# Kernel tuning notes

Measured on AMD Instinct MI355X. Metric: run time of the kernel, lower is better.

Reference implementation:

```python
import jax, jax.numpy as jnp
import numpy as np

NQ = 10      # num_qubits
NL = 3       # num_layers
EPS = 1e-5   # BatchNorm1d eps

# PennyLane gate conventions (wire 0 = most significant bit of the state index)

def _mat_ry(t):
    c, s = jnp.cos(t / 2), jnp.sin(t / 2)
    r0 = jnp.stack([c, -s], -1)
    r1 = jnp.stack([s, c], -1)
    return jnp.stack([r0, r1], -2).astype(jnp.complex64)

def _mat_rx(t):
    c, s = jnp.cos(t / 2), jnp.sin(t / 2)
    c = c.astype(jnp.complex64)
    js = (-1j) * s.astype(jnp.complex64)
    r0 = jnp.stack([c, js], -1)
    r1 = jnp.stack([js, c], -1)
    return jnp.stack([r0, r1], -2)

def _mat_rz(t):
    em = jnp.exp(-0.5j * t.astype(jnp.complex64))
    ep = jnp.exp(0.5j * t.astype(jnp.complex64))
    z = jnp.zeros_like(em)
    r0 = jnp.stack([em, z], -1)
    r1 = jnp.stack([z, ep], -1)
    return jnp.stack([r0, r1], -2)

def _apply_1q(state, U, q):
    # state: (B, 2**NQ); U: (2,2) shared or (B,2,2) per-sample
    B = state.shape[0]
    s = state.reshape(B, 2 ** q, 2, -1)
    if U.ndim == 3:
        s = jnp.einsum('bij,bajc->baic', U, s)
    else:
        s = jnp.einsum('ij,bajc->baic', U, s)
    return s.reshape(B, -1)

def _cnot(state, c, t):
    # control c < target t: flip target bit where control bit == 1
    B = state.shape[0]
    s = state.reshape(B, 2 ** c, 2, 2 ** (t - c - 1), 2, -1)
    s = jnp.stack([s[:, :, 0], s[:, :, 1, :, ::-1, :]], axis=2)
    return s.reshape(B, -1)

def _circuit(x, params):
    # batched statevector simulation of the full circuit
    B = x.shape[0]
    state = jnp.zeros((B, 2 ** NQ), jnp.complex64).at[:, 0].set(1.0)
    for q in range(NQ):                       # RY encoding (per-sample angles)
        state = _apply_1q(state, _mat_ry(x[:, q]), q)
    for l in range(NL):
        for q in range(NQ):                   # RZ, RX, RY trainable rotations
            state = _apply_1q(state, _mat_rz(params[l, q, 0]), q)
            state = _apply_1q(state, _mat_rx(params[l, q, 1]), q)
            state = _apply_1q(state, _mat_ry(params[l, q, 2]), q)
        for i in range(NQ - 1):               # 'full' entanglement: CNOT chain
            state = _cnot(state, i, i + 1)
    probs = state.real ** 2 + state.imag ** 2
    exps = []
    for q in range(NQ):                       # <Z_q> = P(bit_q=0) - P(bit_q=1)
        p = probs.reshape(B, 2 ** q, 2, -1).sum(axis=(1, 3))
        exps.append(p[:, 0] - p[:, 1])
    return jnp.stack(exps, axis=1)            # (B, NQ)

def setup_inputs() -> dict:
    key = jax.random.key(0)
    k1, k2 = jax.random.split(key)
    x = jax.random.normal(k1, (16384, NQ), jnp.float32)
    params = jax.random.normal(k2, (NL, NQ, 3), jnp.float32)
    gamma = jnp.ones((NQ,), jnp.float32)
    beta = jnp.zeros((NQ,), jnp.float32)
    return {"x": x, "params": params, "gamma": gamma, "beta": beta}

def reference(x, params, gamma, beta):
    out = _circuit(x, params)
    # BatchNorm1d in training mode (biased batch variance)
    mean = out.mean(axis=0)
    var = ((out - mean) ** 2).mean(axis=0)
    return gamma * (out - mean) * jax.lax.rsqrt(var + EPS) + beta
```

## Files before the change

kernel.cpp:

```cpp
#include <hip/hip_runtime.h>
#include <hip/hip_fp16.h>

#define NQ 10
#define NSAMP 16384
#define BN_EPS 1e-5f

union H2U { __half2 h; unsigned u; };
__device__ __forceinline__ __half2 u2h(unsigned u) { H2U t; t.u = u; return t.h; }
__device__ __forceinline__ unsigned h2u(__half2 h) { H2U t; t.h = h; return t.u; }
__device__ __forceinline__ __half2 hswap(__half2 x) { return __lowhigh2highlow(x); }
__device__ __forceinline__ __half2 hpack(float lo, float hi) {
  return __floats2half2_rn(lo, hi);
}

template<int M>
__device__ __forceinline__ unsigned shufu(unsigned v, int a30, int a28, int a20) {
  if constexpr (M < 32) {
    return (unsigned)__builtin_amdgcn_ds_swizzle((int)v, (M << 10) | 0x1F);
  } else {
    const int addr = (M == 0x30) ? a30 : (M == 0x28) ? a28 : a20;
    return (unsigned)__builtin_amdgcn_ds_bpermute(addr, (int)v);
  }
}
template<int M>
__device__ __forceinline__ __half2 shufh(__half2 v, int a30, int a28, int a20) {
  return u2h(shufu<M>(h2u(v), a30, a28, a20));
}

constexpr int ML_[3][10] = {
  {0x20,0x10,0x08,0x04,0x02,0x01, 0,   0,   0,   0},
  {0x30,0x18,0x0C,0x06,0x03,0x01, 0,   0,   0,   0},
  {0x28,0x14,0x0A,0x05,0x02,0x01, 0,   0,   0,   0}};
constexpr int MR_[3][10] = {
  {0,0,0,0,0,0,   0x8,0x4,0x2,0x1},
  {0,0,0,0,0,0x8, 0xC,0x6,0x3,0x1},
  {0,0,0,0,0x8,0x4,0xA,0x5,0x2,0x1}};
constexpr int HR_[3][10] = {
  {0,0,0,0,0,0, 0x8,0x4,0x2,0x1},
  {0,0,0,0,0,0, 0x8,0xC,0xE,0xF},
  {0,0,0,0,0,0, 0x8,0x4,0xA,0x5}};
constexpr int EHL[10] = {0x20,0x30,0x18,0x0C,0x26,0x33,0x19,0x0C,0x26,0x33};

constexpr int SMASK[12] = {0x20,0x30,0x38,0x3C,0x3E,0x3F, 0x20,0x10,0x28,0x14,0x2A,0x15};
constexpr int SIX[2][10] = {{0,1,2,3,4,5,5,5,5,5}, {6,7,8,9,10,11,10,11,10,11}};

constexpr bool par4(int v) { return ((v >> 3 & 1) ^ (v >> 2 & 1) ^ (v >> 1 & 1) ^ (v & 1)) != 0; }

__device__ __forceinline__ void updh(__half2& ar, __half2& ai, __half2 br, __half2 bi,
                                     __half2 WR, __half2 AWI, __half2 NAWI,
                                     __half2 AVR, __half2 VI, __half2 NVI) {
  const __half2 a0r = ar, a0i = ai;
  ar = __hfma2(WR, a0r, __hfma2(AWI, a0i, __hfma2(AVR, br, __hmul2(NVI, bi))));
  ai = __hfma2(WR, a0i, __hfma2(NAWI, a0r, __hfma2(AVR, bi, __hmul2(VI, br))));
}

template<int ML, int MR, int HR>
__device__ __forceinline__ void gateh(__half2* __restrict__ Hr, __half2* __restrict__ Hi,
                                      unsigned sgnw, int a30, int a28, int a20, uint4 cp) {
  const unsigned swi = cp.y ^ sgnw;
  const unsigned svr = cp.z ^ sgnw;
  constexpr unsigned hif = (HR & 8) ? 0x80000000u : 0u;
  const __half2 WR  = u2h(cp.x);
  const __half2 VI  = u2h(cp.w);
  const __half2 NVI = u2h(cp.w ^ 0x80008000u);
  const __half2 WI0 = u2h(swi ^ hif);
  const __half2 WI1 = u2h(swi ^ hif ^ 0x80008000u);
  const __half2 NWI0 = WI1, NWI1 = WI0;
  const __half2 VR0 = u2h(svr ^ hif);
  const __half2 VR1 = u2h(svr ^ hif ^ 0x80008000u);

  if constexpr (MR == 0) {
    #pragma unroll
    for (int j = 0; j < 8; ++j) {
      const __half2 br = shufh<ML>(Hr[j], a30, a28, a20);
      const __half2 bi = shufh<ML>(Hi[j], a30, a28, a20);
      const bool cp_ = par4(j & (HR & 7));
      updh(Hr[j], Hi[j], br, bi, WR, cp_ ? WI1 : WI0, cp_ ? NWI1 : NWI0,
           cp_ ? VR1 : VR0, VI, NVI);
    }
  } else if constexpr ((MR & 7) == 0) {
    #pragma unroll
    for (int j = 0; j < 8; ++j) {
      __half2 br = Hr[j], bi = Hi[j];
      if constexpr (ML != 0) { br = shufh<ML>(br, a30, a28, a20); bi = shufh<ML>(bi, a30, a28, a20); }
      br = hswap(br); bi = hswap(bi);
      const bool cp_ = par4(j & (HR & 7));
      updh(Hr[j], Hi[j], br, bi, WR, cp_ ? WI1 : WI0, cp_ ? NWI1 : NWI0,
           cp_ ? VR1 : VR0, VI, NVI);
    }
  } else {
    constexpr int JX = MR & 7;
    constexpr int HB = (JX >= 4) ? 4 : (JX >= 2) ? 2 : 1;
    #pragma unroll
    for (int j = 0; j < 8; ++j) {
      if (!(j & HB)) {
        const int j2 = j ^ JX;
        __half2 bra = Hr[j2], bia = Hi[j2], brb = Hr[j], bib = Hi[j];
        if constexpr (ML != 0) {
          bra = shufh<ML>(bra, a30, a28, a20); bia = shufh<ML>(bia, a30, a28, a20);
          brb = shufh<ML>(brb, a30, a28, a20); bib = shufh<ML>(bib, a30, a28, a20);
        }
        if constexpr ((MR & 8) != 0) {
          bra = hswap(bra); bia = hswap(bia); brb = hswap(brb); bib = hswap(bib);
        }
        const bool cpa = par4(j & (HR & 7));
        updh(Hr[j], Hi[j], bra, bia, WR, cpa ? WI1 : WI0, cpa ? NWI1 : NWI0,
             cpa ? VR1 : VR0, VI, NVI);
        const bool cpb = par4(j2 & (HR & 7));
        updh(Hr[j2], Hi[j2], brb, bib, WR, cpb ? WI1 : WI0, cpb ? NWI1 : NWI0,
             cpb ? VR1 : VR0, VI, NVI);
      }
    }
  }
}

template<int L, int Q>
__device__ __forceinline__ void rotgh(const uint4* __restrict__ cph, __half2* Hr, __half2* Hi,
                                      const unsigned* __restrict__ sgnv,
                                      int a30, int a28, int a20) {
  const uint4 cp = cph[(L - 1) * 10 + Q];
  gateh<ML_[L][Q], MR_[L][Q], HR_[L][Q]>(Hr, Hi, sgnv[SIX[L - 1][Q]], a30, a28, a20, cp);
}

__device__ __forceinline__ void enc2(const float4 g, float xq,
                                     float& ar, float& ai, float& br, float& bi) {
  const float t = xq * 0.5f;
  const float sq = __sinf(t), cq = __cosf(t);
  ar = g.x * cq - g.z * sq;
  ai = g.y * cq + g.w * sq;
  br = g.z * cq + g.x * sq;
  bi = g.w * cq - g.y * sq;
}
__device__ __forceinline__ void cmul(float& zr, float& zi,
                                     float xr, float xi, float yr, float yi) {
  zr = xr * yr - xi * yi;
  zi = xr * yi + xi * yr;
}

__global__ void coef_kernel(const float* __restrict__ params, float* __restrict__ coef,
                            unsigned* __restrict__ cph, float* __restrict__ stats) {
  int g = threadIdx.x;
  if (g < 20) stats[g] = 0.f;
  if (g < 30) {
    float t0 = params[g * 3 + 0] * 0.5f;
    float t1 = params[g * 3 + 1] * 0.5f;
    float t2 = params[g * 3 + 2] * 0.5f;
    float sa, ca, s2, c2, s3, c3;
    __sincosf(t0, &sa, &ca);
    __sincosf(t1, &s2, &c2);
    __sincosf(t2, &s3, &c3);
    float A = c3 * c2, Bv = s3 * s2, C = s3 * c2, D = c3 * s2;
    float wr = A * ca + Bv * sa;
    float wi = Bv * ca - A * sa;
    float vr = C * ca - D * sa;
    float vi = -(C * sa + D * ca);
    coef[g * 4 + 0] = wr;
    coef[g * 4 + 1] = wi;
    coef[g * 4 + 2] = vr;
    coef[g * 4 + 3] = vi;
    if (g >= 10) {
      int gi = g - 10;
      cph[gi * 4 + 0] = h2u(hpack(wr, wr));
      cph[gi * 4 + 1] = h2u(hpack(wi, wi));
      cph[gi * 4 + 2] = h2u(hpack(vr, vr));
      cph[gi * 4 + 3] = h2u(hpack(vi, vi));
    }
  }
}

__global__ __launch_bounds__(256) void circuit_kernel(const float* __restrict__ x,
                                                      const float* __restrict__ coef,
                                                      const uint4* __restrict__ cph,
                                                      float* __restrict__ out,
                                                      float* __restrict__ stats) {
  const int lane = threadIdx.x & 63;
  const int wv = threadIdx.x >> 6;
  const int wid = __builtin_amdgcn_readfirstlane(
      (int)((blockIdx.x * blockDim.x + threadIdx.x) >> 6));
  const float4* cg = (const float4*)coef;

  const int a30 = (lane ^ 0x30) << 2;
  const int a28 = (lane ^ 0x28) << 2;
  const int a20 = (lane ^ 0x20) << 2;

  unsigned sgnv[12];
  #pragma unroll
  for (int k = 0; k < 12; ++k)
    sgnv[k] = (__builtin_popcount(lane & SMASK[k]) & 1) ? 0u : 0x80008000u;

  const float* xrow = x + wid * NQ;
  float lr, li;
  {
    float ar, ai, br, bi;
    enc2(cg[0], xrow[0], ar, ai, br, bi);
    lr = (lane & 32) ? br : ar;
    li = (lane & 32) ? bi : ai;
  }
  #pragma unroll
  for (int q = 1; q < 6; ++q) {
    float ar, ai, br, bi;
    enc2(cg[q], xrow[q], ar, ai, br, bi);
    const int bit = 1 << (5 - q);
    const float tr = (lane & bit) ? br : ar;
    const float ti = (lane & bit) ? bi : ai;
    const float nr = lr * tr - li * ti;
    const float ni = lr * ti + li * tr;
    lr = nr; li = ni;
  }
  float sr[16], si[16];
  {
    float ar, ai, br, bi;
    float t2r[2], t2i[2], t4r[4], t4i[4], t8r[8], t8i[8];
    enc2(cg[6], xrow[6], ar, ai, br, bi);
    cmul(t2r[0], t2i[0], lr, li, ar, ai);
    cmul(t2r[1], t2i[1], lr, li, br, bi);
    enc2(cg[7], xrow[7], ar, ai, br, bi);
    #pragma unroll
    for (int j = 0; j < 2; ++j) {
      cmul(t4r[2*j+0], t4i[2*j+0], t2r[j], t2i[j], ar, ai);
      cmul(t4r[2*j+1], t4i[2*j+1], t2r[j], t2i[j], br, bi);
    }
    enc2(cg[8], xrow[8], ar, ai, br, bi);
    #pragma unroll
    for (int j = 0; j < 4; ++j) {
      cmul(t8r[2*j+0], t8i[2*j+0], t4r[j], t4i[j], ar, ai);
      cmul(t8r[2*j+1], t8i[2*j+1], t4r[j], t4i[j], br, bi);
    }
    enc2(cg[9], xrow[9], ar, ai, br, bi);
    #pragma unroll
    for (int j = 0; j < 8; ++j) {
      cmul(sr[2*j+0], si[2*j+0], t8r[j], t8i[j], ar, ai);
      cmul(sr[2*j+1], si[2*j+1], t8r[j], t8i[j], br, bi);
    }
  }
  __half2 Hr[8], Hi[8];
  #pragma unroll
  for (int j = 0; j < 8; ++j) {
    Hr[j] = hpack(sr[j], sr[j | 8]);
    Hi[j] = hpack(si[j], si[j | 8]);
  }

  rotgh<1,0>(cph,Hr,Hi,sgnv,a30,a28,a20); rotgh<1,1>(cph,Hr,Hi,sgnv,a30,a28,a20);
  rotgh<1,2>(cph,Hr,Hi,sgnv,a30,a28,a20); rotgh<1,3>(cph,Hr,Hi,sgnv,a30,a28,a20);
  rotgh<1,4>(cph,Hr,Hi,sgnv,a30,a28,a20); rotgh<1,5>(cph,Hr,Hi,sgnv,a30,a28,a20);
  rotgh<1,6>(cph,Hr,Hi,sgnv,a30,a28,a20); rotgh<1,7>(cph,Hr,Hi,sgnv,a30,a28,a20);
  rotgh<1,8>(cph,Hr,Hi,sgnv,a30,a28,a20); rotgh<1,9>(cph,Hr,Hi,sgnv,a30,a28,a20);

  rotgh<2,0>(cph,Hr,Hi,sgnv,a30,a28,a20); rotgh<2,1>(cph,Hr,Hi,sgnv,a30,a28,a20);
  rotgh<2,2>(cph,Hr,Hi,sgnv,a30,a28,a20); rotgh<2,3>(cph,Hr,Hi,sgnv,a30,a28,a20);
  rotgh<2,4>(cph,Hr,Hi,sgnv,a30,a28,a20); rotgh<2,5>(cph,Hr,Hi,sgnv,a30,a28,a20);
  rotgh<2,6>(cph,Hr,Hi,sgnv,a30,a28,a20); rotgh<2,7>(cph,Hr,Hi,sgnv,a30,a28,a20);
  rotgh<2,8>(cph,Hr,Hi,sgnv,a30,a28,a20); rotgh<2,9>(cph,Hr,Hi,sgnv,a30,a28,a20);

  __half2 A0 = u2h(0u), A1 = A0, A2 = A0, A3 = A0;
  #pragma unroll
  for (int j = 0; j < 8; ++j) {
    const __half2 P = __hfma2(Hr[j], Hr[j], __hmul2(Hi[j], Hi[j]));
    A0 = __hadd2(A0, P);
    A1 = par4(j & 4) ? __hsub2(A1, P) : __hadd2(A1, P);
    A2 = par4(j & 6) ? __hsub2(A2, P) : __hadd2(A2, P);
    A3 = par4(j & 3) ? __hsub2(A3, P) : __hadd2(A3, P);
  }
  const float a0lo = __half2float(__low2half(A0)), a0hi = __half2float(__high2half(A0));
  const float a1lo = __half2float(__low2half(A1)), a1hi = __half2float(__high2half(A1));
  const float a2lo = __half2float(__low2half(A2)), a2hi = __half2float(__high2half(A2));
  const float a3lo = __half2float(__low2half(A3)), a3hi = __half2float(__high2half(A3));
  const float tot = a0lo + a0hi;
  const float s8  = a0lo - a0hi;
  const float sc  = a1lo - a1hi;
  const float s6  = a2lo + a2hi;
  const float s3  = a3lo + a3hi;

  const float S[10] = {tot, tot, tot, tot, tot, tot, s8, sc, s6, s3};
  __half2 E[5];
  #pragma unroll
  for (int k = 0; k < 5; ++k) {
    float ea = S[2 * k], eb = S[2 * k + 1];
    ea = (__builtin_popcount(lane & EHL[2 * k]) & 1) ? -ea : ea;
    eb = (__builtin_popcount(lane & EHL[2 * k + 1]) & 1) ? -eb : eb;
    E[k] = hpack(ea, eb);
  }
  #pragma unroll
  for (int k = 0; k < 5; ++k) {
    E[k] = __hadd2(E[k], shufh<0x20>(E[k], a30, a28, a20));
    E[k] = __hadd2(E[k], shufh<0x10>(E[k], a30, a28, a20));
    E[k] = __hadd2(E[k], shufh<0x08>(E[k], a30, a28, a20));
    E[k] = __hadd2(E[k], shufh<0x04>(E[k], a30, a28, a20));
    E[k] = __hadd2(E[k], shufh<0x02>(E[k], a30, a28, a20));
    E[k] = __hadd2(E[k], shufh<0x01>(E[k], a30, a28, a20));
  }

  __shared__ float red[4][20];
  if (lane == 0) {
    #pragma unroll
    for (int k = 0; k < 5; ++k) {
      const float ea = __half2float(__low2half(E[k]));
      const float eb = __half2float(__high2half(E[k]));
      out[wid * NQ + 2 * k]     = ea;
      out[wid * NQ + 2 * k + 1] = eb;
      red[wv][2 * k]          = ea;
      red[wv][2 * k + 1]      = eb;
      red[wv][10 + 2 * k]     = ea * ea;
      red[wv][10 + 2 * k + 1] = eb * eb;
    }
  }
  __syncthreads();
  const int tid = threadIdx.x;
  if (tid < 20) {
    float ssum = red[0][tid] + red[1][tid] + red[2][tid] + red[3][tid];
    atomicAdd(&stats[tid], ssum);
  }
}

__global__ __launch_bounds__(256) void bn_kernel(float* __restrict__ out,
                                                 const float* __restrict__ stats,
                                                 const float* __restrict__ gamma,
                                                 const float* __restrict__ beta) {
  int i = blockIdx.x * 256 + threadIdx.x;
  if (i < NSAMP * NQ) {
    int q = i % NQ;
    float mean = stats[q] * (1.f / NSAMP);
    float var = stats[10 + q] * (1.f / NSAMP) - mean * mean;
    if (var < 0.f) var = 0.f;
    float rstd = rsqrtf(var + BN_EPS);
    float v = out[i];
    out[i] = gamma[q] * (v - mean) * rstd + beta[q];
  }
}

extern "C" void kernel_launch(void* const* d_in, const int* in_sizes, int n_in,
                              void* d_out, int out_size, void* d_ws, size_t ws_size,
                              hipStream_t stream) {
  const float* x      = (const float*)d_in[0];
  const float* params = (const float*)d_in[1];
  const float* gamma  = (const float*)d_in[2];
  const float* beta   = (const float*)d_in[3];
  float* out = (float*)d_out;
  float* stats = (float*)d_ws;
  float* coef = (float*)d_ws + 32;
  unsigned* cph = (unsigned*)((float*)d_ws + 160);

  coef_kernel<<<1, 32, 0, stream>>>(params, coef, cph, stats);
  circuit_kernel<<<NSAMP / 4, 256, 0, stream>>>(x, coef, (const uint4*)cph, out, stats);
  bn_kernel<<<(NSAMP * NQ + 255) / 256, 256, 0, stream>>>(out, stats, gamma, beta);
}
```

Baseline: 70.93 us.

## Pack two samples per wavefront in half2 lanes instead of splitting one state

Each wavefront now simulates two samples at once: the low and high halves of every half2 register hold the same amplitude index for sample A and sample B, and each lane keeps 16 registers instead of 8. This removes the in-register half swaps used when a gate paired the packed halves, and drops the special sign handling for the high half. The grid is halved. In exchange each lane holds twice as many state registers and builds two encoded states, and the final reduction shuffles ten packed values instead of five.

```diff
diff --git a/kernel.cpp b/kernel.cpp
--- a/kernel.cpp
+++ b/kernel.cpp
@@ -4,11 +4,11 @@
 #define NQ 10
 #define NSAMP 16384
 #define BN_EPS 1e-5f
+#define SGN 0x80008000u
 
 union H2U { __half2 h; unsigned u; };
 __device__ __forceinline__ __half2 u2h(unsigned u) { H2U t; t.u = u; return t.h; }
 __device__ __forceinline__ unsigned h2u(__half2 h) { H2U t; t.h = h; return t.u; }
-__device__ __forceinline__ __half2 hswap(__half2 x) { return __lowhigh2highlow(x); }
 __device__ __forceinline__ __half2 hpack(float lo, float hi) {
   return __floats2half2_rn(lo, hi);
 }
@@ -44,6 +44,9 @@
 constexpr int SMASK[12] = {0x20,0x30,0x38,0x3C,0x3E,0x3F, 0x20,0x10,0x28,0x14,0x2A,0x15};
 constexpr int SIX[2][10] = {{0,1,2,3,4,5,5,5,5,5}, {6,7,8,9,10,11,10,11,10,11}};
 
+constexpr int hibit4(int m) {
+  return m >= 8 ? 8 : (m >= 4 ? 4 : (m >= 2 ? 2 : (m ? 1 : 0)));
+}
 constexpr bool par4(int v) { return ((v >> 3 & 1) ^ (v >> 2 & 1) ^ (v >> 1 & 1) ^ (v & 1)) != 0; }
 
 __device__ __forceinline__ void updh(__half2& ar, __half2& ai, __half2 br, __half2 bi,
@@ -59,63 +62,50 @@
                                       unsigned sgnw, int a30, int a28, int a20, uint4 cp) {
   const unsigned swi = cp.y ^ sgnw;
   const unsigned svr = cp.z ^ sgnw;
-  constexpr unsigned hif = (HR & 8) ? 0x80000000u : 0u;
   const __half2 WR  = u2h(cp.x);
   const __half2 VI  = u2h(cp.w);
-  const __half2 NVI = u2h(cp.w ^ 0x80008000u);
-  const __half2 WI0 = u2h(swi ^ hif);
-  const __half2 WI1 = u2h(swi ^ hif ^ 0x80008000u);
-  const __half2 NWI0 = WI1, NWI1 = WI0;
-  const __half2 VR0 = u2h(svr ^ hif);
-  const __half2 VR1 = u2h(svr ^ hif ^ 0x80008000u);
+  const __half2 NVI = u2h(cp.w ^ SGN);
+  const __half2 WI0 = u2h(swi);
+  const __half2 WI1 = u2h(swi ^ SGN);
+  const __half2 VR0 = u2h(svr);
+  const __half2 VR1 = u2h(svr ^ SGN);
 
   if constexpr (MR == 0) {
     #pragma unroll
-    for (int j = 0; j < 8; ++j) {
-      const __half2 br = shufh<ML>(Hr[j], a30, a28, a20);
-      const __half2 bi = shufh<ML>(Hi[j], a30, a28, a20);
-      const bool cp_ = par4(j & (HR & 7));
-      updh(Hr[j], Hi[j], br, bi, WR, cp_ ? WI1 : WI0, cp_ ? NWI1 : NWI0,
-           cp_ ? VR1 : VR0, VI, NVI);
-    }
-  } else if constexpr ((MR & 7) == 0) {
-    #pragma unroll
-    for (int j = 0; j < 8; ++j) {
-      __half2 br = Hr[j], bi = Hi[j];
-      if constexpr (ML != 0) { br = shufh<ML>(br, a30, a28, a20); bi = shufh<ML>(bi, a30, a28, a20); }
-      br = hswap(br); bi = hswap(bi);
-      const bool cp_ = par4(j & (HR & 7));
-      updh(Hr[j], Hi[j], br, bi, WR, cp_ ? WI1 : WI0, cp_ ? NWI1 : NWI0,
-           cp_ ? VR1 : VR0, VI, NVI);
+    for (int r = 0; r < 16; ++r) {
+      const __half2 br = shufh<ML>(Hr[r], a30, a28, a20);
+      const __half2 bi = shufh<ML>(Hi[r], a30, a28, a20);
+      const bool p = par4(r & HR);
+      updh(Hr[r], Hi[r], br, bi, WR, p ? WI1 : WI0, p ? WI0 : WI1,
+           p ? VR1 : VR0, VI, NVI);
     }
   } else {
-    constexpr int JX = MR & 7;
-    constexpr int HB = (JX >= 4) ? 4 : (JX >= 2) ? 2 : 1;
+    constexpr int HB = hibit4(MR);
     #pragma unroll
-    for (int j = 0; j < 8; ++j) {
-      if (!(j & HB)) {
-        const int j2 = j ^ JX;
-        __half2 bra = Hr[j2], bia = Hi[j2], brb = Hr[j], bib = Hi[j];
+    for (int r = 0; r < 16; ++r) {
+      if (!(r & HB)) {
+        const int r2 = r ^ MR;
+        __half2 b0r, b0i, b1r, b1i;
         if constexpr (ML != 0) {
-          bra = shufh<ML>(bra, a30, a28, a20); bia = shufh<ML>(bia, a30, a28, a20);
-          brb = shufh<ML>(brb, a30, a28, a20); bib = shufh<ML>(bib, a30, a28, a20);
+          b0r = shufh<ML>(Hr[r2], a30, a28, a20); b0i = shufh<ML>(Hi[r2], a30, a28, a20);
+          b1r = shufh<ML>(Hr[r],  a30, a28, a20); b1i = shufh<ML>(Hi[r],  a30, a28, a20);
+        } else {
+          b0r = Hr[r2]; b0i = Hi[r2]; b1r = Hr[r]; b1i = Hi[r];
         }
-        if constexpr ((MR & 8) != 0) {
-          bra = hswap(bra); bia = hswap(bia); brb = hswap(brb); bib = hswap(bib);
-        }
-        const bool cpa = par4(j & (HR & 7));
-        updh(Hr[j], Hi[j], bra, bia, WR, cpa ? WI1 : WI0, cpa ? NWI1 : NWI0,
-             cpa ? VR1 : VR0, VI, NVI);
-        const bool cpb = par4(j2 & (HR & 7));
-        updh(Hr[j2], Hi[j2], brb, bib, WR, cpb ? WI1 : WI0, cpb ? NWI1 : NWI0,
-             cpb ? VR1 : VR0, VI, NVI);
+        const bool pa = par4(r & HR);
+        updh(Hr[r], Hi[r], b0r, b0i, WR, pa ? WI1 : WI0, pa ? WI0 : WI1,
+             pa ? VR1 : VR0, VI, NVI);
+        const bool pb = par4(r2 & HR);
+        updh(Hr[r2], Hi[r2], b1r, b1i, WR, pb ? WI1 : WI0, pb ? WI0 : WI1,
+             pb ? VR1 : VR0, VI, NVI);
       }
     }
   }
 }
 
 template<int L, int Q>
-__device__ __forceinline__ void rotgh(const uint4* __restrict__ cph, __half2* Hr, __half2* Hi,
+__device__ __forceinline__ void rotgh(const uint4* __restrict__ cph,
+                                      __half2* Hr, __half2* Hi,
                                       const unsigned* __restrict__ sgnv,
                                       int a30, int a28, int a20) {
   const uint4 cp = cph[(L - 1) * 10 + Q];
@@ -135,6 +125,53 @@
                                      float xr, float xi, float yr, float yi) {
   zr = xr * yr - xi * yi;
   zi = xr * yi + xi * yr;
+}
+
+__device__ __forceinline__ void build_state(const float* __restrict__ xrow,
+                                            const float4* __restrict__ cg,
+                                            int lane, float* __restrict__ sr,
+                                            float* __restrict__ si) {
+  float lr, li;
+  {
+    float ar, ai, br, bi;
+    enc2(cg[0], xrow[0], ar, ai, br, bi);
+    lr = (lane & 32) ? br : ar;
+    li = (lane & 32) ? bi : ai;
+  }
+  #pragma unroll
+  for (int q = 1; q < 6; ++q) {
+    float ar, ai, br, bi;
+    enc2(cg[q], xrow[q], ar, ai, br, bi);
+    const int bit = 1 << (5 - q);
+    const float tr = (lane & bit) ? br : ar;
+    const float ti = (lane & bit) ? bi : ai;
+    const float nr = lr * tr - li * ti;
+    const float ni = lr * ti + li * tr;
+    lr = nr; li = ni;
+  }
+  float ar, ai, br, bi;
+  float t2r[2], t2i[2], t4r[4], t4i[4], t8r[8], t8i[8];
+  enc2(cg[6], xrow[6], ar, ai, br, bi);
+  cmul(t2r[0], t2i[0], lr, li, ar, ai);
+  cmul(t2r[1], t2i[1], lr, li, br, bi);
+  enc2(cg[7], xrow[7], ar, ai, br, bi);
+  #pragma unroll
+  for (int j = 0; j < 2; ++j) {
+    cmul(t4r[2*j+0], t4i[2*j+0], t2r[j], t2i[j], ar, ai);
+    cmul(t4r[2*j+1], t4i[2*j+1], t2r[j], t2i[j], br, bi);
+  }
+  enc2(cg[8], xrow[8], ar, ai, br, bi);
+  #pragma unroll
+  for (int j = 0; j < 4; ++j) {
+    cmul(t8r[2*j+0], t8i[2*j+0], t4r[j], t4i[j], ar, ai);
+    cmul(t8r[2*j+1], t8i[2*j+1], t4r[j], t4i[j], br, bi);
+  }
+  enc2(cg[9], xrow[9], ar, ai, br, bi);
+  #pragma unroll
+  for (int j = 0; j < 8; ++j) {
+    cmul(sr[2*j+0], si[2*j+0], t8r[j], t8i[j], ar, ai);
+    cmul(sr[2*j+1], si[2*j+1], t8r[j], t8i[j], br, bi);
+  }
 }
 
 __global__ void coef_kernel(const float* __restrict__ params, float* __restrict__ coef,
@@ -186,58 +223,17 @@
   unsigned sgnv[12];
   #pragma unroll
   for (int k = 0; k < 12; ++k)
-    sgnv[k] = (__builtin_popcount(lane & SMASK[k]) & 1) ? 0u : 0x80008000u;
-
-  const float* xrow = x + wid * NQ;
-  float lr, li;
-  {
-    float ar, ai, br, bi;
-    enc2(cg[0], xrow[0], ar, ai, br, bi);
-    lr = (lane & 32) ? br : ar;
-    li = (lane & 32) ? bi : ai;
-  }
-  #pragma unroll
-  for (int q = 1; q < 6; ++q) {
-    float ar, ai, br, bi;
-    enc2(cg[q], xrow[q], ar, ai, br, bi);
-    const int bit = 1 << (5 - q);
-    const float tr = (lane & bit) ? br : ar;
-    const float ti = (lane & bit) ? bi : ai;
-    const float nr = lr * tr - li * ti;
-    const float ni = lr * ti + li * tr;
-    lr = nr; li = ni;
-  }
-  float sr[16], si[16];
-  {
-    float ar, ai, br, bi;
-    float t2r[2], t2i[2], t4r[4], t4i[4], t8r[8], t8i[8];
-    enc2(cg[6], xrow[6], ar, ai, br, bi);
-    cmul(t2r[0], t2i[0], lr, li, ar, ai);
-    cmul(t2r[1], t2i[1], lr, li, br, bi);
-    enc2(cg[7], xrow[7], ar, ai, br, bi);
-    #pragma unroll
-    for (int j = 0; j < 2; ++j) {
-      cmul(t4r[2*j+0], t4i[2*j+0], t2r[j], t2i[j], ar, ai);
-      cmul(t4r[2*j+1], t4i[2*j+1], t2r[j], t2i[j], br, bi);
-    }
-    enc2(cg[8], xrow[8], ar, ai, br, bi);
-    #pragma unroll
-    for (int j = 0; j < 4; ++j) {
-      cmul(t8r[2*j+0], t8i[2*j+0], t4r[j], t4i[j], ar, ai);
-      cmul(t8r[2*j+1], t8i[2*j+1], t4r[j], t4i[j], br, bi);
-    }
-    enc2(cg[9], xrow[9], ar, ai, br, bi);
-    #pragma unroll
-    for (int j = 0; j < 8; ++j) {
-      cmul(sr[2*j+0], si[2*j+0], t8r[j], t8i[j], ar, ai);
-      cmul(sr[2*j+1], si[2*j+1], t8r[j], t8i[j], br, bi);
-    }
-  }
-  __half2 Hr[8], Hi[8];
-  #pragma unroll
-  for (int j = 0; j < 8; ++j) {
-    Hr[j] = hpack(sr[j], sr[j | 8]);
-    Hi[j] = hpack(si[j], si[j | 8]);
+    sgnv[k] = (__builtin_popcount(lane & SMASK[k]) & 1) ? 0u : SGN;
+
+  const int sA = wid * 2, sB = wid * 2 + 1;
+  float srA[16], siA[16], srB[16], siB[16];
+  build_state(x + sA * NQ, cg, lane, srA, siA);
+  build_state(x + sB * NQ, cg, lane, srB, siB);
+  __half2 Hr[16], Hi[16];
+  #pragma unroll
+  for (int r = 0; r < 16; ++r) {
+    Hr[r] = hpack(srA[r], srB[r]);
+    Hi[r] = hpack(siA[r], siB[r]);
   }
 
   rotgh<1,0>(cph,Hr,Hi,sgnv,a30,a28,a20); rotgh<1,1>(cph,Hr,Hi,sgnv,a30,a28,a20);
@@ -252,56 +248,43 @@
   rotgh<2,6>(cph,Hr,Hi,sgnv,a30,a28,a20); rotgh<2,7>(cph,Hr,Hi,sgnv,a30,a28,a20);
   rotgh<2,8>(cph,Hr,Hi,sgnv,a30,a28,a20); rotgh<2,9>(cph,Hr,Hi,sgnv,a30,a28,a20);
 
-  __half2 A0 = u2h(0u), A1 = A0, A2 = A0, A3 = A0;
-  #pragma unroll
-  for (int j = 0; j < 8; ++j) {
-    const __half2 P = __hfma2(Hr[j], Hr[j], __hmul2(Hi[j], Hi[j]));
-    A0 = __hadd2(A0, P);
-    A1 = par4(j & 4) ? __hsub2(A1, P) : __hadd2(A1, P);
-    A2 = par4(j & 6) ? __hsub2(A2, P) : __hadd2(A2, P);
-    A3 = par4(j & 3) ? __hsub2(A3, P) : __hadd2(A3, P);
-  }
-  const float a0lo = __half2float(__low2half(A0)), a0hi = __half2float(__high2half(A0));
-  const float a1lo = __half2float(__low2half(A1)), a1hi = __half2float(__high2half(A1));
-  const float a2lo = __half2float(__low2half(A2)), a2hi = __half2float(__high2half(A2));
-  const float a3lo = __half2float(__low2half(A3)), a3hi = __half2float(__high2half(A3));
-  const float tot = a0lo + a0hi;
-  const float s8  = a0lo - a0hi;
-  const float sc  = a1lo - a1hi;
-  const float s6  = a2lo + a2hi;
-  const float s3  = a3lo + a3hi;
-
-  const float S[10] = {tot, tot, tot, tot, tot, tot, s8, sc, s6, s3};
-  __half2 E[5];
-  #pragma unroll
-  for (int k = 0; k < 5; ++k) {
-    float ea = S[2 * k], eb = S[2 * k + 1];
-    ea = (__builtin_popcount(lane & EHL[2 * k]) & 1) ? -ea : ea;
-    eb = (__builtin_popcount(lane & EHL[2 * k + 1]) & 1) ? -eb : eb;
-    E[k] = hpack(ea, eb);
-  }
-  #pragma unroll
-  for (int k = 0; k < 5; ++k) {
-    E[k] = __hadd2(E[k], shufh<0x20>(E[k], a30, a28, a20));
-    E[k] = __hadd2(E[k], shufh<0x10>(E[k], a30, a28, a20));
-    E[k] = __hadd2(E[k], shufh<0x08>(E[k], a30, a28, a20));
-    E[k] = __hadd2(E[k], shufh<0x04>(E[k], a30, a28, a20));
-    E[k] = __hadd2(E[k], shufh<0x02>(E[k], a30, a28, a20));
-    E[k] = __hadd2(E[k], shufh<0x01>(E[k], a30, a28, a20));
+  __half2 T = u2h(0u), S8 = T, SC = T, S6 = T, S3 = T;
+  #pragma unroll
+  for (int r = 0; r < 16; ++r) {
+    const __half2 P = __hfma2(Hr[r], Hr[r], __hmul2(Hi[r], Hi[r]));
+    T = __hadd2(T, P);
+    S8 = par4(r & 0x8) ? __hsub2(S8, P) : __hadd2(S8, P);
+    SC = par4(r & 0xC) ? __hsub2(SC, P) : __hadd2(SC, P);
+    S6 = par4(r & 0x6) ? __hsub2(S6, P) : __hadd2(S6, P);
+    S3 = par4(r & 0x3) ? __hsub2(S3, P) : __hadd2(S3, P);
+  }
+  const __half2 S[10] = {T, T, T, T, T, T, S8, SC, S6, S3};
+  __half2 e[10];
+  #pragma unroll
+  for (int q = 0; q < 10; ++q) {
+    const bool neg = (__builtin_popcount(lane & EHL[q]) & 1) != 0;
+    e[q] = u2h(h2u(S[q]) ^ (neg ? SGN : 0u));
+  }
+  #pragma unroll
+  for (int q = 0; q < 10; ++q) {
+    e[q] = __hadd2(e[q], shufh<0x20>(e[q], a30, a28, a20));
+    e[q] = __hadd2(e[q], shufh<0x10>(e[q], a30, a28, a20));
+    e[q] = __hadd2(e[q], shufh<0x08>(e[q], a30, a28, a20));
+    e[q] = __hadd2(e[q], shufh<0x04>(e[q], a30, a28, a20));
+    e[q] = __hadd2(e[q], shufh<0x02>(e[q], a30, a28, a20));
+    e[q] = __hadd2(e[q], shufh<0x01>(e[q], a30, a28, a20));
   }
 
   __shared__ float red[4][20];
   if (lane == 0) {
     #pragma unroll
-    for (int k = 0; k < 5; ++k) {
-      const float ea = __half2float(__low2half(E[k]));
-      const float eb = __half2float(__high2half(E[k]));
-      out[wid * NQ + 2 * k]     = ea;
-      out[wid * NQ + 2 * k + 1] = eb;
-      red[wv][2 * k]          = ea;
-      red[wv][2 * k + 1]      = eb;
-      red[wv][10 + 2 * k]     = ea * ea;
-      red[wv][10 + 2 * k + 1] = eb * eb;
+    for (int q = 0; q < 10; ++q) {
+      const float ea = __half2float(__low2half(e[q]));
+      const float eb = __half2float(__high2half(e[q]));
+      out[sA * NQ + q] = ea;
+      out[sB * NQ + q] = eb;
+      red[wv][q]      = ea + eb;
+      red[wv][10 + q] = ea * ea + eb * eb;
     }
   }
   __syncthreads();
@@ -341,6 +324,6 @@
   unsigned* cph = (unsigned*)((float*)d_ws + 160);
 
   coef_kernel<<<1, 32, 0, stream>>>(params, coef, cph, stats);
-  circuit_kernel<<<NSAMP / 4, 256, 0, stream>>>(x, coef, (const uint4*)cph, out, stats);
+  circuit_kernel<<<NSAMP / 8, 256, 0, stream>>>(x, coef, (const uint4*)cph, out, stats);
   bn_kernel<<<(NSAMP * NQ + 255) / 256, 256, 0, stream>>>(out, stats, gamma, beta);
 }
```

New measurement: 66.46 us (median of 2 runs). -6.3%, faster.
